# Optimization experiments

Measured on AMD Instinct MI355X. Metric: run time of the kernel, lower is better.

## Reference

```python
import jax, jax.numpy as jnp
import numpy as np
import math

# ---- Cl(3,0) algebra tables; blade order sorted by grade: 1, e1,e2,e3, e12,e13,e23, e123 ----
def _build_algebra():
    d = 3
    masks = sorted(range(1 << d), key=lambda m: (bin(m).count('1'), m))
    idx = {m: i for i, m in enumerate(masks)}
    cay = np.zeros((8, 8, 8), dtype=np.float32)
    for a in range(8):
        for b in range(8):
            t, cnt = a >> 1, 0
            while t:
                cnt += bin(t & b).count('1')
                t >>= 1
            s = -1.0 if (cnt & 1) else 1.0  # Euclidean metric: repeated generators square to +1
            cay[idx[a], idx[a ^ b], idx[b]] = s  # cayley[i,j,k]: (e_i e_k) component on e_j
    grades = np.array([bin(m).count('1') for m in masks])
    slices = [np.where(grades == g)[0] for g in range(d + 1)]
    paths = np.zeros((d + 1,) * 3, dtype=bool)
    for i in range(d + 1):
        for j in range(d + 1):
            for k in range(d + 1):
                paths[i, j, k] = bool(np.any(cay[np.ix_(slices[i], slices[j], slices[k])] != 0))
    return cay, paths, grades

CAYLEY, PATHS, SUB_IDX = _build_algebra()  # SUB_IDX: blade -> grade-subspace index [0,1,1,1,2,2,2,3]
PATH_IDX = np.argwhere(PATHS)              # [P,3] nonzero grade-product paths (P=20 for Cl(3,0))
P = PATH_IDX.shape[0]
SQRT2 = math.sqrt(2.0)
EPS = 1e-6
B, N = 65536, 16


def _qs(x):
    # per-grade quadratic form (mag2): [..., 8] -> [..., 4]; Euclidean => sum of squares per grade
    x2 = x * x
    return jnp.stack([x2[..., 0], x2[..., 1:4].sum(-1), x2[..., 4:7].sum(-1), x2[..., 7]], axis=-1)


def _mv_linear(x, w, b=None):
    # x: [B, n, 8]; w: [m, n, 4] (one weight per grade subspace); bias on scalar blade
    wf = w[..., SUB_IDX]  # expand per-grade weights to per-blade: [m, n, 8]
    out = jnp.einsum('bni,mni->bmi', x, wf)
    if b is not None:
        out = out.at[..., 0].add(b)
    return out


def _geometric_product_layer(x, w_right, a_norm, w_gp, w_left, b_left):
    xr = _mv_linear(x, w_right)  # linear_right, no bias
    # NormalizationLayer (init=0): gated rescale toward unit per-grade norm
    nr = jnp.sqrt(_qs(xr))                              # [B, n, 4]
    nr = jax.nn.sigmoid(a_norm) * (nr - 1.0) + 1.0
    xr = xr / (nr[..., SUB_IDX] + EPS)
    # scatter sparse path weights into dense [m, n, 4, 4, 4] grade tensor
    m, n = w_left.shape[0], w_left.shape[1]
    wd = jnp.zeros((m, n, 4, 4, 4), w_gp.dtype).at[:, :, PATH_IDX[:, 0], PATH_IDX[:, 1], PATH_IDX[:, 2]].set(w_gp)
    # expand grades -> blades and weight the Cayley table: [m, n, 8, 8, 8]
    wb = wd[:, :, SUB_IDX][:, :, :, SUB_IDX][:, :, :, :, SUB_IDX] * CAYLEY
    gp = jnp.einsum('bni,mnijk,bnk->bmj', x, wb, xr)
    return (_mv_linear(x, w_left, b_left) + gp) / SQRT2


def _mv_silu(x, a, b):
    # invariants: scalar blade itself + mag2 of grades 1..3, affine, gate all blades of each grade
    inv = jnp.concatenate([x[..., :1], _qs(x)[..., 1:]], axis=-1)  # [B, c, 4]
    gate = jax.nn.sigmoid((a * inv + b)[..., SUB_IDX])
    return gate * x


def setup_inputs() -> dict:
    key = jax.random.key(0)
    ks = jax.random.split(key, 8)
    s = 1.0 / math.sqrt(N * 4)
    return {
        'x': jax.random.normal(ks[0], (B, N, 8), jnp.float32),
        'w_right': jax.random.normal(ks[1], (N, N, 4), jnp.float32) * s,
        'a_norm': jnp.zeros((1, N, 4), jnp.float32),
        'w_gp': jax.random.normal(ks[2], (N, N, P), jnp.float32) * s,
        'w_left': jax.random.normal(ks[3], (N, N, 4), jnp.float32) * s,
        'b_left': jnp.zeros((N,), jnp.float32),
        'w_up': jax.random.normal(ks[4], (4 * N, N, 4), jnp.float32) * s,
        'b_up': jnp.zeros((4 * N,), jnp.float32),
        'a_act': jnp.ones((1, 4 * N, 4), jnp.float32),
        'b_act': jnp.zeros((1, 4 * N, 4), jnp.float32),
        'w_down': jax.random.normal(ks[5], (N, 4 * N, 4), jnp.float32) * (1.0 / math.sqrt(4 * N * 4)),
        'b_down': jnp.zeros((N,), jnp.float32),
    }


def reference(x, w_right, a_norm, w_gp, w_left, b_left, w_up, b_up, a_act, b_act, w_down, b_down):
    attended = _geometric_product_layer(x, w_right, a_norm, w_gp, w_left, b_left)
    h = _mv_linear(attended, w_up, b_up)
    h = _mv_silu(h, a_act, b_act)
    h = _mv_linear(h, w_down, b_down)
    return attended + h
```

## Files before the change

kernel.cpp:

```cpp
#include <hip/hip_runtime.h>
#include <hip/hip_bf16.h>
#include <math.h>

#define TPB 512
#define XS    132
#define OFF_X  0
#define OFF_XR 8448
#define XRU4   2112
#define SMEM_FLOATS (8448 + 4352)
#define SMEM_BYTES  (SMEM_FLOATS * 4)

constexpr int SCNT[44] = {1,1,1,1,1,1,1,1, 3,1,1,1, 2,2,2,2,2,2, 1,1,1, 3,
                          3, 2,2,2, 1,1,1,1,1,1, 2,2,2, 3, 1,1,1,1,1,1,1,1};
constexpr int T1I[44] = {0,0,0,0,0,0,0,0, 1,1,2,3, 2,1,1,1,1,2, 3,2,1, 1,
                         4, 4,4,5, 6,5,4,4,5,6, 5,4,4, 4, 7,7,7,7,7,7,7,7};
constexpr int T1K[44] = {0,1,2,3,4,5,6,7, 1,0,0,0, 4,4,5,2,3,3, 7,7,7, 6,
                         4, 2,1,1, 7,7,7,0,0,0, 6,6,5, 3, 7,6,5,4,3,2,1,0};
constexpr int T1S[44] = {1,1,1,1,1,1,1,1, 1,1,1,1, 0,1,1,1,1,1, 1,0,1, 1,
                         0, 1,0,0, 0,1,0,1,1,1, 0,1,0, 1, 0,0,1,0,1,0,1,1};
constexpr int T2I[44] = {0,0,0,0,0,0,0,0, 2,0,0,0, 3,3,2,2,3,3, 0,0,0, 2,
                         5, 5,6,6, 0,0,0,0,0,0, 6,6,5, 5, 0,0,0,0,0,0,0,0};
constexpr int T2K[44] = {0,0,0,0,0,0,0,0, 2,0,0,0, 5,6,6,1,1,2, 0,0,0, 5,
                         5, 3,3,2, 0,0,0,0,0,0, 5,4,4, 2, 0,0,0,0,0,0,0,0};
constexpr int T2S[44] = {1,1,1,1,1,1,1,1, 1,1,1,1, 0,0,1,0,0,0, 1,1,1, 0,
                         0, 1,1,0, 1,1,1,1,1,1, 1,0,1, 0, 1,1,1,1,1,1,1,1};
constexpr int T3I[44] = {0,0,0,0,0,0,0,0, 3,0,0,0, 0,0,0,0,0,0, 0,0,0, 3,
                         6, 0,0,0, 0,0,0,0,0,0, 0,0,0, 6, 0,0,0,0,0,0,0,0};
constexpr int T3K[44] = {0,0,0,0,0,0,0,0, 3,0,0,0, 0,0,0,0,0,0, 0,0,0, 4,
                         6, 0,0,0, 0,0,0,0,0,0, 0,0,0, 1, 0,0,0,0,0,0,0,0};
constexpr int T3S[44] = {1,1,1,1,1,1,1,1, 1,1,1,1, 1,1,1,1,1,1, 1,1,1, 1,
                         0, 1,1,1, 1,1,1,1,1,1, 1,1,1, 1, 1,1,1,1,1,1,1,1};
constexpr int CP[44] = {
    0, 1,1,1, 2,2,2, 3,
    4, 5,5,5, 6,6,6, 7,7,7, 8,8,8, 9,
    10, 11,11,11, 12,12,12, 13,13,13, 14,14,14, 15,
    16, 17,17,17, 18,18,18, 19};
constexpr int PPS2[30][2] = {
    {0,8},{22,36},{44,52}, {1,9},{12,23},{26,37},{45,52}, {2,10},{13,24},{27,38},{46,52},
    {3,11},{14,25},{28,39},{47,52},
    {4,15},{18,29},{32,40},{48,52}, {5,16},{19,30},{33,41},{49,52}, {6,17},{20,31},{34,42},{50,52},
    {7,21},{35,43},{51,52}};
constexpr int FRS2[30] = {0,0,0, 1,1,1,1, 2,2,2,2, 3,3,3,3,  0,0,0,0, 1,1,1,1, 2,2,2,2, 3,3,3};

typedef __attribute__((ext_vector_type(8))) short bf16x8;
typedef __attribute__((ext_vector_type(4))) float f32x4;
union U4B { uint4 u; bf16x8 h; };

__device__ __forceinline__ float sigmoidf_(float v) {
    return __builtin_amdgcn_rcpf(1.0f + __expf(-v));
}
__device__ __forceinline__ unsigned pk2(float lo, float hi) {
    __hip_bfloat162 h = __float22bfloat162_rn(make_float2(lo, hi));
    return *reinterpret_cast<unsigned*>(&h);
}
__device__ __forceinline__ void unpkrow(uint4 u, float* v) {
    v[0]=__uint_as_float(u.x<<16); v[1]=__uint_as_float(u.x&0xffff0000u);
    v[2]=__uint_as_float(u.y<<16); v[3]=__uint_as_float(u.y&0xffff0000u);
    v[4]=__uint_as_float(u.z<<16); v[5]=__uint_as_float(u.z&0xffff0000u);
    v[6]=__uint_as_float(u.w<<16); v[7]=__uint_as_float(u.w&0xffff0000u);
}

template<int S>
__device__ __forceinline__ float tz_slot(const float* xf, const float* xr) {
    if constexpr (S >= 52) {
        return 0.0f;
    } else if constexpr (S >= 44) {
        return xf[S - 44];
    } else {
        float v = xf[T1I[S]] * xr[T1K[S]];
        if constexpr (!T1S[S]) v = -v;
        if constexpr (SCNT[S] > 1) {
            if constexpr (T2S[S]) v = fmaf( xf[T2I[S]], xr[T2K[S]], v);
            else                  v = fmaf(-xf[T2I[S]], xr[T2K[S]], v);
        }
        if constexpr (SCNT[S] > 2) {
            if constexpr (T3S[S]) v = fmaf( xf[T3I[S]], xr[T3K[S]], v);
            else                  v = fmaf(-xf[T3I[S]], xr[T3K[S]], v);
        }
        return v;
    }
}

template<int JH, int P, int HALF>
__device__ __forceinline__ void gp_half(const float (&xf)[2][8], const float (&xrf)[2][8],
                                        const uint4* __restrict__ wsg, int lane,
                                        f32x4 (&cf)[4]) {
    if constexpr (P < 15) {
        constexpr int Q  = JH*15 + P;
        constexpr int S0 = PPS2[Q][0], S1 = PPS2[Q][1], F = FRS2[Q];
        const unsigned d0 = pk2(tz_slot<S0>(xf[0], xrf[0]), tz_slot<S1>(xf[0], xrf[0]));
        const unsigned d1 = pk2(tz_slot<S0>(xf[1], xrf[1]), tz_slot<S1>(xf[1], xrf[1]));
        U4B a;
        if constexpr (HALF == 0) { a.u = make_uint4(d0, d1, 0u, 0u); }
        else                     { a.u = make_uint4(0u, 0u, d0, d1); }
        U4B wb; wb.u = wsg[Q*64 + lane];
        cf[F] = __builtin_amdgcn_mfma_f32_16x16x32_bf16(a.h, wb.h, cf[F], 0, 0, 0);
        gp_half<JH, P+1, HALF>(xf, xrf, wsg, lane, cf);
    }
}

__global__ void prep_pack(const float* __restrict__ w_up,
                          const float* __restrict__ w_down,
                          const float* __restrict__ w_gp,
                          const float* __restrict__ w_left,
                          const float* __restrict__ w_right,
                          unsigned* __restrict__ wsu,
                          unsigned* __restrict__ wsd,
                          uint4* __restrict__ wsg,
                          uint4* __restrict__ wsr)
{
    const int t = blockIdx.x * 256 + threadIdx.x;
    if (t < 8192) {
        const int d  = t;
        const int f  = d >> 8;
        const int rj = d & 255;
        const int l  = rj >> 2, jp = rj & 3;
        const int mt = f >> 3, i = f & 7;
        const int g  = (i == 0) ? 0 : (i <= 3 ? 1 : (i <= 6 ? 2 : 3));
        const int rho = l & 15;
        const int m2 = 32*(mt>>1) + 4*(mt&1) + 8*(rho>>2) + (rho&3);
        const int n0 = ((l >> 4) << 3) + (jp << 1);
        const float v0 = (n0     < 16) ? w_up[(m2*16 + n0    )*4 + g] : 0.f;
        const float v1 = (n0 + 1 < 16) ? w_up[(m2*16 + n0 + 1)*4 + g] : 0.f;
        wsu[d] = pk2(v0, v1);
    } else if (t < 12288) {
        const int d  = t - 8192;
        const int f  = d >> 8;
        const int rj = d & 255;
        const int l  = rj >> 2, jp = rj & 3;
        const int kt = f >> 3, i = f & 7;
        const int g  = (i == 0) ? 0 : (i <= 3 ? 1 : (i <= 6 ? 2 : 3));
        const int m  = l & 15;
        const int k0 = 32*kt + ((l >> 4) << 3) + (jp << 1);
        wsd[d] = pk2(w_down[(m*64 + k0    )*4 + g],
                     w_down[(m*64 + k0 + 1)*4 + g]);
    } else if (t < 14208) {
        const int u = t - 12288;
        const int l = u & 63, q = u >> 6;
        const int m = l & 15, lh = l >> 4;
        const int s0 = PPS2[q][0], s1 = PPS2[q][1];
        auto wslot = [&](int S, int n) -> float {
            if (S >= 52) return 0.f;
            if (S >= 44) {
                const int j = S - 44;
                const int gg = (j == 0) ? 0 : (j <= 3 ? 1 : (j <= 6 ? 2 : 3));
                return w_left[(m*16 + n)*4 + gg];
            }
            return w_gp[(m*16 + n)*20 + CP[S]];
        };
        uint4 val;
        { const int n = 4*lh + 0; val.x = pk2(wslot(s0, n), wslot(s1, n)); }
        { const int n = 4*lh + 1; val.y = pk2(wslot(s0, n), wslot(s1, n)); }
        { const int n = 4*lh + 2; val.z = pk2(wslot(s0, n), wslot(s1, n)); }
        { const int n = 4*lh + 3; val.w = pk2(wslot(s0, n), wslot(s1, n)); }
        wsg[q*64 + l] = val;
    } else if (t < 14720) {
        const int u2 = t - 14208;
        const int l = u2 & 63, j = u2 >> 6;
        const int g  = (j == 0) ? 0 : (j <= 3 ? 1 : (j <= 6 ? 2 : 3));
        const int nch = l & 15;
        const int lh2 = l >> 4;
        uint4 val = make_uint4(0u,0u,0u,0u);
        if (lh2 < 2) {
            const int kb = 8*lh2;
            val.x = pk2(w_right[(nch*16+kb+0)*4+g], w_right[(nch*16+kb+1)*4+g]);
            val.y = pk2(w_right[(nch*16+kb+2)*4+g], w_right[(nch*16+kb+3)*4+g]);
            val.z = pk2(w_right[(nch*16+kb+4)*4+g], w_right[(nch*16+kb+5)*4+g]);
            val.w = pk2(w_right[(nch*16+kb+6)*4+g], w_right[(nch*16+kb+7)*4+g]);
        }
        wsr[j*64 + l] = val;
    }
}

__global__ __launch_bounds__(TPB, 4)
void mv_block_kernel(const float* __restrict__ xg,
                     const float* __restrict__ a_norm,
                     const float* __restrict__ b_left,
                     const float* __restrict__ b_up,
                     const float* __restrict__ a_act,
                     const float* __restrict__ b_act,
                     const float* __restrict__ b_down,
                     const uint4* __restrict__ wsu,
                     const uint4* __restrict__ wsd,
                     const uint4* __restrict__ wsg,
                     const uint4* __restrict__ wsr,
                     float* __restrict__ outg)
{
    extern __shared__ float sm[];
    uint4* uXR = ((uint4*)sm) + XRU4;
    const int t = threadIdx.x;
    const int b = t & 63;
    const int w = __builtin_amdgcn_readfirstlane(t >> 6);
    const int mA = 2*w, mB = 2*w + 1;
    const int g = blockIdx.x;
    const int Mtb  = (w & 3) << 4;
    const int jh   = w >> 2;
    const int lcol = b & 15;
    const int lh   = b >> 4;

    {
        const float4* xs = (const float4*)xg + (size_t)g * 2048;
        #pragma unroll
        for (int r = 0; r < 4; ++r) {
            const int idx = r * TPB + t;
            const float4 v = xs[idx];
            const int el = idx >> 5, off = idx & 31;
            *(float4*)&sm[OFF_X + el * XS + off * 4] = v;
        }
    }
    __syncthreads();

    {
        uint4 Bf[4];
        #pragma unroll
        for (int q = 0; q < 4; ++q) Bf[q] = make_uint4(0u,0u,0u,0u);
        if (lh < 2) {
            float4 xk[8];
            const float* xb = &sm[OFF_X + (Mtb + lcol)*XS + (jh<<2)];
            #pragma unroll
            for (int kk = 0; kk < 8; ++kk)
                xk[kk] = *(const float4*)&xb[(8*lh + kk)*8];
            Bf[0] = make_uint4(pk2(xk[0].x,xk[1].x), pk2(xk[2].x,xk[3].x),
                               pk2(xk[4].x,xk[5].x), pk2(xk[6].x,xk[7].x));
            Bf[1] = make_uint4(pk2(xk[0].y,xk[1].y), pk2(xk[2].y,xk[3].y),
                               pk2(xk[4].y,xk[5].y), pk2(xk[6].y,xk[7].y));
            Bf[2] = make_uint4(pk2(xk[0].z,xk[1].z), pk2(xk[2].z,xk[3].z),
                               pk2(xk[4].z,xk[5].z), pk2(xk[6].z,xk[7].z));
            Bf[3] = make_uint4(pk2(xk[0].w,xk[1].w), pk2(xk[2].w,xk[3].w),
                               pk2(xk[4].w,xk[5].w), pk2(xk[6].w,xk[7].w));
        }
        f32x4 ur[4];
        #pragma unroll
        for (int q = 0; q < 4; ++q) {
            U4B a;  a.u  = wsr[((jh<<2) + q)*64 + b];
            U4B bb; bb.u = Bf[q];
            f32x4 z; z[0]=0.f; z[1]=0.f; z[2]=0.f; z[3]=0.f;
            ur[q] = __builtin_amdgcn_mfma_f32_16x16x32_bf16(a.h, bb.h, z, 0, 0, 0);
        }
        unsigned* uw = (unsigned*)(sm + OFF_XR);
        #pragma unroll
        for (int r = 0; r < 4; ++r) {
            const int nch = 4*lh + r;
            const float4 an = *(const float4*)&a_norm[nch*4];
            float v0 = ur[0][r], v1 = ur[1][r], v2 = ur[2][r], v3 = ur[3][r];
            if (jh == 0) {
                const float i0 = __builtin_amdgcn_rcpf(
                    sigmoidf_(an.x)*(sqrtf(v0*v0)-1.0f)+1.0f + 1e-6f);
                const float i1 = __builtin_amdgcn_rcpf(
                    sigmoidf_(an.y)*(sqrtf(v1*v1+v2*v2+v3*v3)-1.0f)+1.0f + 1e-6f);
                v0*=i0; v1*=i1; v2*=i1; v3*=i1;
            } else {
                const float i2 = __builtin_amdgcn_rcpf(
                    sigmoidf_(an.z)*(sqrtf(v0*v0+v1*v1+v2*v2)-1.0f)+1.0f + 1e-6f);
                const float i3 = __builtin_amdgcn_rcpf(
                    sigmoidf_(an.w)*(sqrtf(v3*v3)-1.0f)+1.0f + 1e-6f);
                v0*=i2; v1*=i2; v2*=i2; v3*=i3;
            }
            const int dwb = (((Mtb + lcol)*17 + nch) << 2) + (jh << 1);
            uw[dwb]     = pk2(v0, v1);
            uw[dwb + 1] = pk2(v2, v3);
        }
    }
    __syncthreads();

    {
        const int brow = Mtb + lcol;
        f32x4 cf[4];
        {
            const float bl = (jh == 0) ? b_left[lcol] : 0.0f;
            cf[0][0]=bl; cf[0][1]=bl; cf[0][2]=bl; cf[0][3]=bl;
            #pragma unroll
            for (int q = 1; q < 4; ++q) { cf[q][0]=0.f; cf[q][1]=0.f; cf[q][2]=0.f; cf[q][3]=0.f; }
        }
        float xf[2][8], xrf[2][8];
        #pragma unroll
        for (int jp = 0; jp < 2; ++jp) {
            const int n = 4*lh + jp;
            const float4 u0 = *(const float4*)&sm[OFF_X + brow*XS + n*8];
            const float4 u1 = *(const float4*)&sm[OFF_X + brow*XS + n*8 + 4];
            xf[jp][0]=u0.x; xf[jp][1]=u0.y; xf[jp][2]=u0.z; xf[jp][3]=u0.w;
            xf[jp][4]=u1.x; xf[jp][5]=u1.y; xf[jp][6]=u1.z; xf[jp][7]=u1.w;
            unpkrow(uXR[brow*17 + n], xrf[jp]);
        }
        if (jh == 0) gp_half<0,0,0>(xf, xrf, wsg, b, cf);
        else         gp_half<1,0,0>(xf, xrf, wsg, b, cf);
        #pragma unroll
        for (int jp = 0; jp < 2; ++jp) {
            const int n = 4*lh + 2 + jp;
            const float4 u0 = *(const float4*)&sm[OFF_X + brow*XS + n*8];
            const float4 u1 = *(const float4*)&sm[OFF_X + brow*XS + n*8 + 4];
            xf[jp][0]=u0.x; xf[jp][1]=u0.y; xf[jp][2]=u0.z; xf[jp][3]=u0.w;
            xf[jp][4]=u1.x; xf[jp][5]=u1.y; xf[jp][6]=u1.z; xf[jp][7]=u1.w;
            unpkrow(uXR[brow*17 + n], xrf[jp]);
        }
        if (jh == 0) gp_half<0,0,1>(xf, xrf, wsg, b, cf);
        else         gp_half<1,0,1>(xf, xrf, wsg, b, cf);
        __syncthreads();
        const float s2 = 0.70710678118654752f;
        #pragma unroll
        for (int r = 0; r < 4; ++r) {
            *(float4*)&sm[OFF_X + (Mtb + 4*lh + r)*XS + (lcol<<3) + (jh<<2)] =
                make_float4(cf[0][r]*s2, cf[1][r]*s2, cf[2][r]*s2, cf[3][r]*s2);
        }
    }
    __syncthreads();

    {
        const float* gx = &sm[OFF_X + b*XS];
        const float4 a0 = *(const float4*)&gx[mA*8];
        const float4 a1 = *(const float4*)&gx[mA*8 + 4];
        const float4 b0 = *(const float4*)&gx[mB*8];
        const float4 b1 = *(const float4*)&gx[mB*8 + 4];
        unsigned* attW = (unsigned*)(sm + OFF_XR);
        const int bsw = b ^ ((w >> 2) << 4);
        attW[(0<<9) + (w<<6) + bsw] = pk2(a0.x, b0.x);
        attW[(1<<9) + (w<<6) + bsw] = pk2(a0.y, b0.y);
        attW[(2<<9) + (w<<6) + bsw] = pk2(a0.z, b0.z);
        attW[(3<<9) + (w<<6) + bsw] = pk2(a0.w, b0.w);
        attW[(4<<9) + (w<<6) + bsw] = pk2(a1.x, b1.x);
        attW[(5<<9) + (w<<6) + bsw] = pk2(a1.y, b1.y);
        attW[(6<<9) + (w<<6) + bsw] = pk2(a1.z, b1.z);
        attW[(7<<9) + (w<<6) + bsw] = pk2(a1.w, b1.w);
    }
    __syncthreads();

    f32x4 dC[4];
    #pragma unroll
    for (int q = 0; q < 4; ++q) { dC[q][0]=0.f; dC[q][1]=0.f; dC[q][2]=0.f; dC[q][3]=0.f; }
    {
        uint4 attB[4];
        {
            const unsigned* aw = (const unsigned*)(sm + OFF_XR);
            #pragma unroll
            for (int q = 0; q < 4; ++q) {
                uint4 v = make_uint4(0u,0u,0u,0u);
                if (lh < 2) {
                    const int base = ((jh*4 + q) << 9);
                    const int bb = (Mtb + lcol) ^ (lh << 4);
                    v.x = aw[base + ((4*lh+0)<<6) + bb];
                    v.y = aw[base + ((4*lh+1)<<6) + bb];
                    v.z = aw[base + ((4*lh+2)<<6) + bb];
                    v.w = aw[base + ((4*lh+3)<<6) + bb];
                }
                attB[q] = v;
            }
        }
        #pragma unroll
        for (int kt = 0; kt < 2; ++kt) {
            unsigned pkl[4][2];
            #pragma unroll
            for (int mte = 0; mte < 2; ++mte) {
                const int mt = 2*kt + mte;
                f32x4 uc[4];
                #pragma unroll
                for (int q = 0; q < 4; ++q) {
                    U4B a;  a.u  = wsu[((mt<<3) + jh*4 + q)*64 + b];
                    U4B bb; bb.u = attB[q];
                    f32x4 z; z[0]=0.f; z[1]=0.f; z[2]=0.f; z[3]=0.f;
                    uc[q] = __builtin_amdgcn_mfma_f32_16x16x32_bf16(a.h, bb.h, z, 0, 0, 0);
                }
                const int m2base = 32*kt + 4*mte + 8*lh;
                const float4 bup4 = *(const float4*)&b_up[m2base];
                const float* bupp = &bup4.x;
                #pragma unroll
                for (int r = 0; r < 4; ++r) {
                    const float4 aa = *(const float4*)&a_act[(m2base + r)*4];
                    const float4 bc = *(const float4*)&b_act[(m2base + r)*4];
                    float h0 = uc[0][r], h1 = uc[1][r], h2 = uc[2][r], h3 = uc[3][r];
                    if (jh == 0) {
                        h0 += bupp[r];
                        const float g0 = sigmoidf_(fmaf(aa.x, h0, bc.x));
                        const float g1 = sigmoidf_(fmaf(aa.y, h1*h1 + h2*h2 + h3*h3, bc.y));
                        h0 *= g0; h1 *= g1; h2 *= g1; h3 *= g1;
                    } else {
                        const float g2 = sigmoidf_(fmaf(aa.z, h0*h0 + h1*h1 + h2*h2, bc.z));
                        const float g3 = sigmoidf_(fmaf(aa.w, h3*h3, bc.w));
                        h0 *= g2; h1 *= g2; h2 *= g2; h3 *= g3;
                    }
                    uc[0][r]=h0; uc[1][r]=h1; uc[2][r]=h2; uc[3][r]=h3;
                }
                if (mte == 0) {
                    #pragma unroll
                    for (int q = 0; q < 4; ++q) {
                        pkl[q][0] = pk2(uc[q][0], uc[q][1]);
                        pkl[q][1] = pk2(uc[q][2], uc[q][3]);
                    }
                } else {
                    #pragma unroll
                    for (int q = 0; q < 4; ++q) {
                        U4B a;
                        a.u.x = pkl[q][0];
                        a.u.y = pkl[q][1];
                        a.u.z = pk2(uc[q][0], uc[q][1]);
                        a.u.w = pk2(uc[q][2], uc[q][3]);
                        U4B wb; wb.u = wsd[((kt<<3) + jh*4 + q)*64 + b];
                        dC[q] = __builtin_amdgcn_mfma_f32_16x16x32_bf16(a.h, wb.h, dC[q], 0, 0, 0);
                    }
                }
            }
        }
    }
    {
        const float bd = (jh == 0) ? b_down[lcol] : 0.0f;
        #pragma unroll
        for (int r = 0; r < 4; ++r) {
            const int br = Mtb + (lh<<2) + r;
            float4 av = *(const float4*)&sm[OFF_X + br*XS + (lcol<<3) + (jh<<2)];
            av.x = (av.x + dC[0][r]) + bd;
            av.y += dC[1][r];
            av.z += dC[2][r];
            av.w += dC[3][r];
            *(float4*)&sm[OFF_X + br*XS + (lcol<<3) + (jh<<2)] = av;
        }
    }
    __syncthreads();

    {
        float4* og = (float4*)outg + (size_t)g * 2048;
        #pragma unroll
        for (int r = 0; r < 4; ++r) {
            const int idx = r * TPB + t;
            const int el = idx >> 5, off = idx & 31;
            og[idx] = *(const float4*)&sm[OFF_X + el * XS + off * 4];
        }
    }
}

extern "C" void kernel_launch(void* const* d_in, const int* in_sizes, int n_in,
                              void* d_out, int out_size, void* d_ws, size_t ws_size,
                              hipStream_t stream) {
    const float* x       = (const float*)d_in[0];
    const float* w_right = (const float*)d_in[1];
    const float* a_norm  = (const float*)d_in[2];
    const float* w_gp    = (const float*)d_in[3];
    const float* w_left  = (const float*)d_in[4];
    const float* b_left  = (const float*)d_in[5];
    const float* w_up    = (const float*)d_in[6];
    const float* b_up    = (const float*)d_in[7];
    const float* a_act   = (const float*)d_in[8];
    const float* b_act   = (const float*)d_in[9];
    const float* w_down  = (const float*)d_in[10];
    const float* b_down  = (const float*)d_in[11];
    float* out = (float*)d_out;

    const int B = in_sizes[0] / 128;
    const int nblocks = B / 64;

    unsigned* wsu = (unsigned*)d_ws;
    unsigned* wsd = wsu + 8192;
    uint4*    wsg = (uint4*)(wsd + 4096);
    uint4*    wsr = wsg + 1920;

    prep_pack<<<58, 256, 0, stream>>>(w_up, w_down, w_gp, w_left, w_right,
                                      wsu, wsd, wsg, wsr);

    (void)hipFuncSetAttribute((const void*)mv_block_kernel,
                              hipFuncAttributeMaxDynamicSharedMemorySize, SMEM_BYTES);
    mv_block_kernel<<<nblocks, TPB, SMEM_BYTES, stream>>>(
        x, a_norm, b_left, b_up, a_act, b_act, b_down,
        (const uint4*)wsu, (const uint4*)wsd, (const uint4*)wsg, (const uint4*)wsr, out);
}
```

Before: 139.7 us.

## Halve block to 32 batch elements with 256 threads for more resident blocks

Shrinks each block from 64 to 32 batch elements and 512 to 256 threads, halving shared memory, and raises the launch-bounds min-blocks hint from 4 to 5. The wave-to-tile mapping and the packed attention-transpose indexing are rewritten for the smaller tile, and twice as many blocks are launched. The aim is higher occupancy and finer scheduling granularity. The cost is lower per-block reuse of weight loads and a tighter register budget, and several hidden sections (the GP and MFMA index mapping) must stay consistent with the new wave count.

```diff
diff --git a/kernel.cpp b/kernel.cpp
--- a/kernel.cpp
+++ b/kernel.cpp
@@ -2,12 +2,12 @@
 #include <hip/hip_bf16.h>
 #include <math.h>
 
-#define TPB 512
+#define TPB 256
 #define XS    132
 #define OFF_X  0
-#define OFF_XR 8448
-#define XRU4   2112
-#define SMEM_FLOATS (8448 + 4352)
+#define OFF_XR 4224
+#define XRU4   1056
+#define SMEM_FLOATS (4224 + 2176)
 #define SMEM_BYTES  (SMEM_FLOATS * 4)
 
 constexpr int SCNT[44] = {1,1,1,1,1,1,1,1, 3,1,1,1, 2,2,2,2,2,2, 1,1,1, 3,
@@ -172,7 +172,7 @@
     }
 }
 
-__global__ __launch_bounds__(TPB, 4)
+__global__ __launch_bounds__(TPB, 5)
 void mv_block_kernel(const float* __restrict__ xg,
                      const float* __restrict__ a_norm,
                      const float* __restrict__ b_left,
@@ -191,15 +191,14 @@
     const int t = threadIdx.x;
     const int b = t & 63;
     const int w = __builtin_amdgcn_readfirstlane(t >> 6);
-    const int mA = 2*w, mB = 2*w + 1;
     const int g = blockIdx.x;
-    const int Mtb  = (w & 3) << 4;
-    const int jh   = w >> 2;
+    const int Mtb  = (w & 1) << 4;
+    const int jh   = w >> 1;
     const int lcol = b & 15;
     const int lh   = b >> 4;
 
     {
-        const float4* xs = (const float4*)xg + (size_t)g * 2048;
+        const float4* xs = (const float4*)xg + (size_t)g * 1024;
         #pragma unroll
         for (int r = 0; r < 4; ++r) {
             const int idx = r * TPB + t;
@@ -306,21 +305,23 @@
     __syncthreads();
 
     {
-        const float* gx = &sm[OFF_X + b*XS];
-        const float4 a0 = *(const float4*)&gx[mA*8];
-        const float4 a1 = *(const float4*)&gx[mA*8 + 4];
-        const float4 b0 = *(const float4*)&gx[mB*8];
-        const float4 b1 = *(const float4*)&gx[mB*8 + 4];
+        const int np = (w << 1) | (b >> 5);
+        const int bt = b & 31;
+        const float* gx = &sm[OFF_X + bt*XS];
+        const float4 a0 = *(const float4*)&gx[np*16];
+        const float4 a1 = *(const float4*)&gx[np*16 + 4];
+        const float4 b0 = *(const float4*)&gx[np*16 + 8];
+        const float4 b1 = *(const float4*)&gx[np*16 + 12];
         unsigned* attW = (unsigned*)(sm + OFF_XR);
-        const int bsw = b ^ ((w >> 2) << 4);
-        attW[(0<<9) + (w<<6) + bsw] = pk2(a0.x, b0.x);
-        attW[(1<<9) + (w<<6) + bsw] = pk2(a0.y, b0.y);
-        attW[(2<<9) + (w<<6) + bsw] = pk2(a0.z, b0.z);
-        attW[(3<<9) + (w<<6) + bsw] = pk2(a0.w, b0.w);
-        attW[(4<<9) + (w<<6) + bsw] = pk2(a1.x, b1.x);
-        attW[(5<<9) + (w<<6) + bsw] = pk2(a1.y, b1.y);
-        attW[(6<<9) + (w<<6) + bsw] = pk2(a1.z, b1.z);
-        attW[(7<<9) + (w<<6) + bsw] = pk2(a1.w, b1.w);
+        const int bsw = bt ^ ((np >> 2) << 4);
+        attW[(0<<8) + (np<<5) + bsw] = pk2(a0.x, b0.x);
+        attW[(1<<8) + (np<<5) + bsw] = pk2(a0.y, b0.y);
+        attW[(2<<8) + (np<<5) + bsw] = pk2(a0.z, b0.z);
+        attW[(3<<8) + (np<<5) + bsw] = pk2(a0.w, b0.w);
+        attW[(4<<8) + (np<<5) + bsw] = pk2(a1.x, b1.x);
+        attW[(5<<8) + (np<<5) + bsw] = pk2(a1.y, b1.y);
+        attW[(6<<8) + (np<<5) + bsw] = pk2(a1.z, b1.z);
+        attW[(7<<8) + (np<<5) + bsw] = pk2(a1.w, b1.w);
     }
     __syncthreads();
 
@@ -335,12 +336,12 @@
             for (int q = 0; q < 4; ++q) {
                 uint4 v = make_uint4(0u,0u,0u,0u);
                 if (lh < 2) {
-                    const int base = ((jh*4 + q) << 9);
+                    const int base = ((jh*4 + q) << 8);
                     const int bb = (Mtb + lcol) ^ (lh << 4);
-                    v.x = aw[base + ((4*lh+0)<<6) + bb];
-                    v.y = aw[base + ((4*lh+1)<<6) + bb];
-                    v.z = aw[base + ((4*lh+2)<<6) + bb];
-                    v.w = aw[base + ((4*lh+3)<<6) + bb];
+                    v.x = aw[base + ((4*lh+0)<<5) + bb];
+                    v.y = aw[base + ((4*lh+1)<<5) + bb];
+                    v.z = aw[base + ((4*lh+2)<<5) + bb];
+                    v.w = aw[base + ((4*lh+3)<<5) + bb];
                 }
                 attB[q] = v;
             }
@@ -416,7 +417,7 @@
     __syncthreads();
 
     {
-        float4* og = (float4*)outg + (size_t)g * 2048;
+        float4* og = (float4*)outg + (size_t)g * 1024;
         #pragma unroll
         for (int r = 0; r < 4; ++r) {
             const int idx = r * TPB + t;
@@ -444,7 +445,7 @@
     float* out = (float*)d_out;
 
     const int B = in_sizes[0] / 128;
-    const int nblocks = B / 64;
+    const int nblocks = B / 32;
 
     unsigned* wsu = (unsigned*)d_ws;
     unsigned* wsd = wsu + 8192;
```

Result: slower. 147.6 us (+5.7%).
